# Kernel tuning notes

Measured on AMD Instinct MI355X. Metric: run time of the kernel, lower is better.

The kernel has to match this reference:

```python
import jax, jax.numpy as jnp
import numpy as np

B, L, D, N = 32, 2048, 1024, 16
N_ITERS = 4
EPS = 1e-8
RMS_EPS = 1e-6
H = 2 * D  # SwiGLU hidden


def setup_inputs() -> dict:
    key = jax.random.key(0)
    ks = jax.random.split(key, 16)
    w = lambda i, shape: jax.random.normal(ks[i], shape, dtype=jnp.float32) * 0.02
    return {
        "encoder_output": jax.random.normal(ks[0], (B, L, D), dtype=jnp.float32),
        "slots_noise": jax.random.normal(ks[1], (B, N, D), dtype=jnp.float32),
        "slots_mu": w(2, (1, 1, D)),
        "slots_sigma": jnp.abs(w(3, (1, 1, D))),
        "g_in": jnp.ones((D,), jnp.float32),     # norm_input.weight
        "g_slots": jnp.ones((D,), jnp.float32),  # norm_slots.weight
        "Wq": w(4, (D, D)),   # torch Linear weight layout (out, in)
        "Wk": w(5, (D, D)),
        "Wv": w(6, (D, D)),
        "w1": w(7, (H, D)),
        "w2": w(8, (H, D)),
        "w3": w(9, (D, H)),
        "W_ih": w(10, (3 * D, D)),  # GRUCell weight_ih (r,z,n stacked)
        "W_hh": w(11, (3 * D, D)),
        "b_ih": jnp.zeros((3 * D,), jnp.float32),
        "b_hh": jnp.zeros((3 * D,), jnp.float32),
    }


def _rmsnorm(x, g):
    var = jnp.mean(x * x, axis=-1, keepdims=True)
    return x * jax.lax.rsqrt(var + RMS_EPS) * g


def _gru_cell(x, h, W_ih, W_hh, b_ih, b_hh):
    # torch.nn.GRUCell: gates ordered (r, z, n)
    gi = x @ W_ih.T + b_ih   # [..., 3D]
    gh = h @ W_hh.T + b_hh
    gi_r, gi_z, gi_n = jnp.split(gi, 3, axis=-1)
    gh_r, gh_z, gh_n = jnp.split(gh, 3, axis=-1)
    r = jax.nn.sigmoid(gi_r + gh_r)
    z = jax.nn.sigmoid(gi_z + gh_z)
    n = jnp.tanh(gi_n + r * gh_n)
    return (1.0 - z) * n + z * h


def reference(encoder_output, slots_noise, slots_mu, slots_sigma, g_in, g_slots,
              Wq, Wk, Wv, w1, w2, w3, W_ih, W_hh, b_ih, b_hh):
    d = encoder_output.shape[-1]
    scale = d ** (-0.5)

    inputs = _rmsnorm(encoder_output, g_in)          # [B, L, D]
    k = inputs @ Wk.T                                # [B, L, D]
    v = inputs @ Wv.T                                # [B, L, D]

    slots = slots_mu + slots_sigma * slots_noise     # [B, N, D]

    for _ in range(N_ITERS):
        slots_prev = slots
        s = _rmsnorm(slots, g_slots)                 # [B, N, D]
        q = s @ Wq.T                                 # [B, N, D]
        dots = jnp.einsum('bnd,bld->bnl', q, k) * scale   # [B, N, L]
        attn = jax.nn.softmax(dots, axis=1)          # competitive softmax over slots
        updates = jnp.einsum('bnl,bld->bnd', attn + EPS, v)     # [B, N, D]
        updates = updates / (jnp.sum(attn, axis=-1, keepdims=True) + EPS)
        # SwiGLU
        updates = (jax.nn.silu(updates @ w1.T) * (updates @ w2.T)) @ w3.T
        slots = _gru_cell(updates, slots_prev, W_ih, W_hh, b_ih, b_hh)
    return slots
```

## Files before the change

### kernel.cpp

```cpp
#include <hip/hip_runtime.h>
#include <hip/hip_bf16.h>
#include <stdint.h>


typedef __bf16 bf16;
typedef __bf16 bf16x4 __attribute__((ext_vector_type(4)));
typedef __bf16 bf16x8 __attribute__((ext_vector_type(8)));
typedef float  f32x2  __attribute__((ext_vector_type(2)));
typedef float  f32x4  __attribute__((ext_vector_type(4)));

#define MFMA16(a,b,c) __builtin_amdgcn_mfma_f32_16x16x32_bf16((a),(b),(c),0,0,0)

__device__ __forceinline__ void gload16(const void* g, void* l) {
  __builtin_amdgcn_global_load_lds((__attribute__((address_space(1))) const void*)g,
                                   (__attribute__((address_space(3))) void*)l, 16, 0, 0);
}

template<int OUT_F32>
__device__ __forceinline__ void g64(const bf16* __restrict__ A, const bf16* __restrict__ B,
                                    void* __restrict__ C, int N, int K,
                                    int brow, int bcol, bf16* As, bf16* Bs)
{
  const int tid = threadIdx.x, wave = tid >> 6, lane = tid & 63;
  const int wm = wave >> 1, wn = wave & 1;
  const int r8 = lane >> 3, c8 = (lane & 7) * 8;
  const int cl = lane & 15, rh = lane >> 4;
  f32x4 acc[2][2] = {};

  const bf16* pa0 = A + (size_t)(brow + wave * 16 + r8) * K + c8;
  const bf16* pa1 = A + (size_t)(brow + wave * 16 + 8 + r8) * K + c8;
  const bf16* pb0 = B + (size_t)(bcol + wave * 16 + r8) * K + c8;
  const bf16* pb1 = B + (size_t)(bcol + wave * 16 + 8 + r8) * K + c8;

  auto ST = [&](int T) {
    const int k0 = T * 64, s = T % 3;
    gload16(pa0 + k0, As + s * 4096 + (wave * 16) * 64);
    gload16(pa1 + k0, As + s * 4096 + (wave * 16 + 8) * 64);
    gload16(pb0 + k0, Bs + s * 4096 + (wave * 16) * 64);
    gload16(pb1 + k0, Bs + s * 4096 + (wave * 16 + 8) * 64);
  };

  const int nt = K >> 6;
  ST(0);
  ST(1);
#pragma unroll 3
  for (int t = 0; t < nt; ++t) {
    __builtin_amdgcn_s_barrier();
    if (t + 2 < nt) {
      ST(t + 2);
      asm volatile("s_waitcnt vmcnt(8)" ::: "memory");
    } else if (t + 1 < nt) {
      asm volatile("s_waitcnt vmcnt(4)" ::: "memory");
    } else {
      asm volatile("s_waitcnt vmcnt(0)" ::: "memory");
    }
    __builtin_amdgcn_sched_barrier(0);
    __builtin_amdgcn_s_barrier();
    const int s = t % 3;
#pragma unroll
    for (int kk = 0; kk < 2; ++kk) {
      bf16x8 af[2], bfv[2];
#pragma unroll
      for (int m = 0; m < 2; ++m)
        af[m] = *(const bf16x8*)(As + s * 4096 + (wm * 32 + m * 16 + cl) * 64 + kk * 32 + rh * 8);
#pragma unroll
      for (int n = 0; n < 2; ++n)
        bfv[n] = *(const bf16x8*)(Bs + s * 4096 + (wn * 32 + n * 16 + cl) * 64 + kk * 32 + rh * 8);
#pragma unroll
      for (int m = 0; m < 2; ++m)
#pragma unroll
        for (int n = 0; n < 2; ++n)
          acc[m][n] = MFMA16(af[m], bfv[n], acc[m][n]);
    }
  }

#pragma unroll
  for (int m = 0; m < 2; ++m)
#pragma unroll
    for (int n = 0; n < 2; ++n) {
      int row0 = brow + wm * 32 + m * 16 + rh * 4;
      int col  = bcol + wn * 32 + n * 16 + cl;
#pragma unroll
      for (int r = 0; r < 4; ++r) {
        if (OUT_F32) ((float*)C)[(size_t)(row0 + r) * N + col] = acc[m][n][r];
        else         ((bf16*)C)[(size_t)(row0 + r) * N + col] = (bf16)acc[m][n][r];
      }
    }
}

template<int OUT_F32>
__global__ __launch_bounds__(256, 3)
void gemm_bt64(const bf16* __restrict__ A0, const bf16* __restrict__ B0, void* __restrict__ C0,
               const bf16* __restrict__ A1, const bf16* __restrict__ B1, void* __restrict__ C1,
               int N, int K0, int K1, float* zbuf)
{
  __shared__ __align__(16) bf16 As[3 * 4096];
  __shared__ __align__(16) bf16 Bs[3 * 4096];
  if (zbuf != nullptr && blockIdx.x == 0 && blockIdx.y == 0 && blockIdx.z == 0) {
    zbuf[threadIdx.x] = 0.f;
    zbuf[threadIdx.x + 256] = 0.f;
  }
  const bf16* A = blockIdx.z ? A1 : A0;
  const bf16* B = blockIdx.z ? B1 : B0;
  void* C = blockIdx.z ? C1 : C0;
  const int K = blockIdx.z ? K1 : K0;
  g64<OUT_F32>(A, B, C, N, K, blockIdx.y * 64, blockIdx.x * 64, As, Bs);
}

__device__ __forceinline__ void g128(const bf16* __restrict__ A, const bf16* __restrict__ B,
                                     bf16* __restrict__ C, int N, int K,
                                     int brow, int bcol, bf16* As, bf16* Bs)
{
  const int tid  = threadIdx.x;
  const int wave = tid >> 6, lane = tid & 63;
  const int wm = wave >> 1, wn = wave & 1;
  const int r_a = lane >> 3, c_a = (lane & 7) * 8;
  const int cl = lane & 15, rh = lane >> 4;

  f32x4 acc[4][4] = {};

  for (int k0 = 0; k0 < K; k0 += 64) {
    __syncthreads();
#pragma unroll
    for (int i = 0; i < 4; ++i) {
      gload16(A + (size_t)(brow + i * 32 + wave * 8 + r_a) * K + k0 + c_a, &As[(i * 32 + wave * 8) * 64]);
      gload16(B + (size_t)(bcol + i * 32 + wave * 8 + r_a) * K + k0 + c_a, &Bs[(i * 32 + wave * 8) * 64]);
    }
    __syncthreads();
#pragma unroll
    for (int kk = 0; kk < 2; ++kk) {
      bf16x8 af[4], bfv[4];
#pragma unroll
      for (int m = 0; m < 4; ++m)
        af[m] = *(const bf16x8*)&As[(wm * 64 + m * 16 + cl) * 64 + kk * 32 + rh * 8];
#pragma unroll
      for (int n = 0; n < 4; ++n)
        bfv[n] = *(const bf16x8*)&Bs[(wn * 64 + n * 16 + cl) * 64 + kk * 32 + rh * 8];
#pragma unroll
      for (int m = 0; m < 4; ++m)
#pragma unroll
        for (int n = 0; n < 4; ++n)
          acc[m][n] = MFMA16(af[m], bfv[n], acc[m][n]);
    }
  }
#pragma unroll
  for (int m = 0; m < 4; ++m)
#pragma unroll
    for (int n = 0; n < 4; ++n) {
      int row0 = brow + wm * 64 + m * 16 + rh * 4;
      int col  = bcol + wn * 64 + n * 16 + cl;
#pragma unroll
      for (int r = 0; r < 4; ++r)
        C[(size_t)(row0 + r) * N + col] = (bf16)acc[m][n][r];
    }
}

__global__ __launch_bounds__(256, 2)
void gemm_pre128(const bf16* __restrict__ wkT, const bf16* __restrict__ wqT, bf16* __restrict__ qm_w,
                 const bf16* __restrict__ w12, const bf16* __restrict__ wvT, bf16* __restrict__ w12v,
                 const bf16* __restrict__ wih, const bf16* __restrict__ w3T, bf16* __restrict__ wih3)
{
  __shared__ __align__(16) bf16 As[128 * 64];
  __shared__ __align__(16) bf16 Bs[128 * 64];
  const int id = blockIdx.x;
  if (id < 64)        g128(wkT, wqT, qm_w, 1024, 1024, (id >> 3) * 128, (id & 7) * 128, As, Bs);
  else if (id < 320) { int t = id - 64;  g128(w12, wvT, w12v, 1024, 1024, (t >> 3) * 128, (t & 7) * 128, As, Bs); }
  else               { int t = id - 320; g128(wih, w3T, wih3, 2048, 1024, (t >> 4) * 128, (t & 15) * 128, As, Bs); }
}

__global__ __launch_bounds__(256, 3)
void gemm_swiglu(const bf16* __restrict__ A, const bf16* __restrict__ B12, bf16* __restrict__ G)
{
  __shared__ __align__(16) bf16 As[2][64 * 64];
  __shared__ __align__(16) bf16 B1s[2][64 * 64];
  __shared__ __align__(16) bf16 B2s[2][64 * 64];
  const int tid = threadIdx.x, wave = tid >> 6, lane = tid & 63;
  const int wm = wave >> 1, wn = wave & 1;
  const int brow = blockIdx.y * 64, bcol = blockIdx.x * 64;
  const int r8 = lane >> 3, c8 = (lane & 7) * 8;
  const int cl = lane & 15, rh = lane >> 4;
  f32x4 acc1[2][2] = {}, acc2[2][2] = {};

  const bf16* pa0 = A   + (size_t)(brow + wave * 16 + r8) * 1024 + c8;
  const bf16* pa1 = A   + (size_t)(brow + wave * 16 + 8 + r8) * 1024 + c8;
  const bf16* p10 = B12 + (size_t)(bcol + wave * 16 + r8) * 1024 + c8;
  const bf16* p11 = B12 + (size_t)(bcol + wave * 16 + 8 + r8) * 1024 + c8;
  const bf16* p20 = B12 + (size_t)(2048 + bcol + wave * 16 + r8) * 1024 + c8;
  const bf16* p21 = B12 + (size_t)(2048 + bcol + wave * 16 + 8 + r8) * 1024 + c8;

#define STSW(T) {                                                   \
    int k0_ = (T) * 64, s_ = (T) & 1;                               \
    gload16(pa0 + k0_, &As[s_][(wave * 16) * 64]);                  \
    gload16(pa1 + k0_, &As[s_][(wave * 16 + 8) * 64]);              \
    gload16(p10 + k0_, &B1s[s_][(wave * 16) * 64]);                 \
    gload16(p11 + k0_, &B1s[s_][(wave * 16 + 8) * 64]);             \
    gload16(p20 + k0_, &B2s[s_][(wave * 16) * 64]);                 \
    gload16(p21 + k0_, &B2s[s_][(wave * 16 + 8) * 64]);             \
  }

  STSW(0)
  for (int t = 0; t < 16; ++t) {
    if (t < 15) {
      STSW(t + 1)
      asm volatile("s_waitcnt vmcnt(6)" ::: "memory");
    } else {
      asm volatile("s_waitcnt vmcnt(0)" ::: "memory");
    }
    __builtin_amdgcn_sched_barrier(0);
    __builtin_amdgcn_s_barrier();
    __builtin_amdgcn_sched_barrier(0);
    const int s = t & 1;
#pragma unroll
    for (int kk = 0; kk < 2; ++kk) {
      bf16x8 af[2], b1v[2], b2v[2];
#pragma unroll
      for (int m = 0; m < 2; ++m)
        af[m] = *(const bf16x8*)&As[s][(wm * 32 + m * 16 + cl) * 64 + kk * 32 + rh * 8];
#pragma unroll
      for (int n = 0; n < 2; ++n) {
        b1v[n] = *(const bf16x8*)&B1s[s][(wn * 32 + n * 16 + cl) * 64 + kk * 32 + rh * 8];
        b2v[n] = *(const bf16x8*)&B2s[s][(wn * 32 + n * 16 + cl) * 64 + kk * 32 + rh * 8];
      }
#pragma unroll
      for (int m = 0; m < 2; ++m)
#pragma unroll
        for (int n = 0; n < 2; ++n) {
          acc1[m][n] = MFMA16(af[m], b1v[n], acc1[m][n]);
          acc2[m][n] = MFMA16(af[m], b2v[n], acc2[m][n]);
        }
    }
    __builtin_amdgcn_sched_barrier(0);
    __builtin_amdgcn_s_barrier();
    __builtin_amdgcn_sched_barrier(0);
  }
#undef STSW

#pragma unroll
  for (int m = 0; m < 2; ++m)
#pragma unroll
    for (int n = 0; n < 2; ++n) {
      int row0 = brow + wm * 32 + m * 16 + rh * 4;
      int col  = bcol + wn * 32 + n * 16 + cl;
#pragma unroll
      for (int r = 0; r < 4; ++r) {
        float h1 = acc1[m][n][r], h2 = acc2[m][n][r];
        G[(size_t)(row0 + r) * 2048 + col] = (bf16)(h1 / (1.f + __expf(-h1)) * h2);
      }
    }
}

__global__ __launch_bounds__(256, 2)
void fused_attn(const bf16* __restrict__ qm, const bf16* __restrict__ x,
                bf16* __restrict__ part, float* __restrict__ attn_sum)
{
  extern __shared__ __align__(16) char smem[];
  char* ss  = smem;
  char* ksl = smem + 32768;
  float* p_lds = (float*)(smem + 65536);

  const int lc = blockIdx.x, b = blockIdx.y;
  const int tid = threadIdx.x, wave = tid >> 6, lane = tid & 63;
  const int cl = lane & 15, rh = lane >> 4;

  const bf16* sb = qm + (size_t)b * 16 * 1024;
  {
    const int c16 = tid & 127, row2 = tid >> 7;
#pragma unroll
    for (int i = 0; i < 8; ++i) {
      int row = i * 2 + row2;
      int colb = (c16 * 16) ^ ((row & 7) << 4);
      gload16(sb + row * 1024 + colb / 2, ss + i * 4096 + wave * 1024);
    }
  }

  const bf16* kb = x + ((size_t)b * 2048 + lc * 128) * 1024;
  const int ksw  = ((lane & 7) ^ ((lane >> 3) & 7)) * 8;
  const int krow = wave * 8 + (lane >> 3);

#define STAGE_KS(KT) {                                                            \
    char* d_ = ksl + ((KT) & 1) * 16384;                                          \
    _Pragma("unroll")                                                             \
    for (int i = 0; i < 4; ++i)                                                   \
      gload16(kb + (size_t)(i * 32 + krow) * 1024 + (KT) * 64 + ksw,              \
              d_ + (i * 32 + wave * 8) * 128);                                    \
  }

  f32x4 acc[2] = {};
  STAGE_KS(0)
  for (int kt = 0; kt < 16; ++kt) {
    if (kt < 15) { STAGE_KS(kt + 1) }
    __builtin_amdgcn_sched_barrier(0);
    if (kt < 15) asm volatile("s_waitcnt vmcnt(4)" ::: "memory");
    else         asm volatile("s_waitcnt vmcnt(0)" ::: "memory");
    __builtin_amdgcn_sched_barrier(0);
    __builtin_amdgcn_s_barrier();
    const char* sbuf = ksl + (kt & 1) * 16384;
#pragma unroll
    for (int kk = 0; kk < 2; ++kk) {
      bf16x8 af = *(const bf16x8*)(ss + cl * 2048 +
                    ((kt * 128 + kk * 64 + rh * 16) ^ ((cl & 7) << 4)));
#pragma unroll
      for (int n = 0; n < 2; ++n) {
        int row = wave * 32 + n * 16 + cl;
        bf16x8 bfv = *(const bf16x8*)(sbuf + row * 128 +
                      ((kk * 64 + rh * 16) ^ ((row & 7) << 4)));
        acc[n] = MFMA16(af, bfv, acc[n]);
      }
    }
    __builtin_amdgcn_s_barrier();
    __builtin_amdgcn_sched_barrier(0);
  }
#undef STAGE_KS

  const float scale = 0.03125f;
  float rs[4] = {0.f, 0.f, 0.f, 0.f};
#pragma unroll
  for (int n = 0; n < 2; ++n) {
    float xv[4];
#pragma unroll
    for (int r = 0; r < 4; ++r) xv[r] = acc[n][r] * scale;
    float mx = fmaxf(fmaxf(xv[0], xv[1]), fmaxf(xv[2], xv[3]));
    mx = fmaxf(mx, __shfl_xor(mx, 16));
    mx = fmaxf(mx, __shfl_xor(mx, 32));
    float e[4], sm = 0.f;
#pragma unroll
    for (int r = 0; r < 4; ++r) { e[r] = __expf(xv[r] - mx); sm += e[r]; }
    sm += __shfl_xor(sm, 16);
    sm += __shfl_xor(sm, 32);
    float inv = 1.f / sm;
    f32x4 pk;
#pragma unroll
    for (int r = 0; r < 4; ++r) { float av = e[r] * inv; rs[r] += av; pk[r] = av; }
    int ll = wave * 32 + n * 16 + cl;
    *(f32x4*)&p_lds[ll * 20 + rh * 4] = pk;
  }
#pragma unroll
  for (int off = 1; off < 16; off <<= 1) {
#pragma unroll
    for (int r = 0; r < 4; ++r) rs[r] += __shfl_xor(rs[r], off);
  }
  if (cl == 0) {
#pragma unroll
    for (int r = 0; r < 4; ++r) atomicAdd(&attn_sum[b * 16 + rh * 4 + r], rs[r]);
  }
  __syncthreads();

  const bf16* vb = x + ((size_t)b * 2048 + lc * 128) * 1024 + tid * 4;
  f32x2 pacc2[8][4] = {};
  for (int l = 0; l < 128; ++l) {
    bf16x4 vv = *(const bf16x4*)(vb + (size_t)l * 1024);
    f32x2 xs[4];
#pragma unroll
    for (int j = 0; j < 4; ++j) { float f = (float)vv[j]; xs[j][0] = f; xs[j][1] = f; }
    f32x2 p2[8];
#pragma unroll
    for (int sp = 0; sp < 8; ++sp) p2[sp] = *(const f32x2*)&p_lds[l * 20 + sp * 2];
#pragma unroll
    for (int sp = 0; sp < 8; ++sp)
#pragma unroll
      for (int j = 0; j < 4; ++j)
        pacc2[sp][j] += p2[sp] * xs[j];
  }
  bf16* pb = part + ((size_t)(lc * 32 + b) * 16) * 1024 + tid * 4;
#pragma unroll
  for (int n = 0; n < 16; ++n) {
    bf16x4 o;
#pragma unroll
    for (int r = 0; r < 4; ++r) o[r] = (bf16)pacc2[n >> 1][r][n & 1];
    *(bf16x4*)(pb + (size_t)n * 1024) = o;
  }
}

__global__ void updates_finalize(const bf16* __restrict__ part, const float* __restrict__ attn_sum,
                                 bf16* __restrict__ updraw)
{
  int idx8 = (blockIdx.x * 256 + threadIdx.x) * 8;
  int m = idx8 >> 10;
  float s[8] = {};
#pragma unroll
  for (int ls = 0; ls < 16; ++ls) {
    bf16x8 v = *(const bf16x8*)(part + idx8 + (size_t)ls * 524288);
#pragma unroll
    for (int j = 0; j < 8; ++j) s[j] += (float)v[j];
  }
  float inv = 1.f / (attn_sum[m] + 1e-8f);
  bf16x8 o;
#pragma unroll
  for (int j = 0; j < 8; ++j) o[j] = (bf16)(s[j] * inv);
  *(bf16x8*)(updraw + idx8) = o;
}

__global__ __launch_bounds__(256)
void gru_pw_fused(const float* __restrict__ gi, const float* __restrict__ gh,
                  const float* __restrict__ bih, const float* __restrict__ bhh,
                  const float* __restrict__ g_sl,
                  float* __restrict__ slots, bf16* __restrict__ slots_bf,
                  bf16* __restrict__ s_bf, float* __restrict__ outp)
{
  const int m = blockIdx.x, tid = threadIdx.x;
  const int d0 = tid * 4;
  const size_t base = (size_t)m * 3072 + d0;
  f32x4 gir = *(const f32x4*)(gi + base),        ghr = *(const f32x4*)(gh + base);
  f32x4 giz = *(const f32x4*)(gi + base + 1024), ghz = *(const f32x4*)(gh + base + 1024);
  f32x4 gin = *(const f32x4*)(gi + base + 2048), ghn = *(const f32x4*)(gh + base + 2048);
  f32x4 br  = *(const f32x4*)(bih + d0),        bhr = *(const f32x4*)(bhh + d0);
  f32x4 bz  = *(const f32x4*)(bih + 1024 + d0), bhz = *(const f32x4*)(bhh + 1024 + d0);
  f32x4 bn  = *(const f32x4*)(bih + 2048 + d0), bhn = *(const f32x4*)(bhh + 2048 + d0);
  f32x4 h   = *(const f32x4*)(slots + (size_t)m * 1024 + d0);
  float o[4]; float ssum = 0.f;
#pragma unroll
  for (int j = 0; j < 4; ++j) {
    float r  = gir[j] + br[j] + ghr[j] + bhr[j];
    float z  = giz[j] + bz[j] + ghz[j] + bhz[j];
    float nn = gin[j] + bn[j];
    float hn = ghn[j] + bhn[j];
    r = 1.f / (1.f + expf(-r));
    z = 1.f / (1.f + expf(-z));
    nn = tanhf(nn + r * hn);
    o[j] = (1.f - z) * nn + z * h[j];
    ssum += o[j] * o[j];
  }
#pragma unroll
  for (int off = 32; off; off >>= 1) ssum += __shfl_xor(ssum, off);
  __shared__ float red[4];
  if ((tid & 63) == 0) red[tid >> 6] = ssum;
  __syncthreads();
  float tot = red[0] + red[1] + red[2] + red[3];
  float rsc = rsqrtf(tot * (1.f / 1024.f) + 1e-6f);
  f32x4 gv = *(const f32x4*)(g_sl + d0);
  f32x4 of; bf16x4 ob, sb;
#pragma unroll
  for (int j = 0; j < 4; ++j) { of[j] = o[j]; ob[j] = (bf16)o[j]; sb[j] = (bf16)(o[j] * rsc * gv[j]); }
  *(f32x4*)(slots + (size_t)m * 1024 + d0) = of;
  *(f32x4*)(outp  + (size_t)m * 1024 + d0) = of;
  *(bf16x4*)(slots_bf + (size_t)m * 1024 + d0) = ob;
  *(bf16x4*)(s_bf     + (size_t)m * 1024 + d0) = sb;
}

__global__ __launch_bounds__(256)
void init_slots_fused(const float* __restrict__ noise, const float* __restrict__ mu,
                      const float* __restrict__ sigma, const float* __restrict__ g_sl,
                      float* __restrict__ slots, bf16* __restrict__ slots_bf,
                      bf16* __restrict__ s_bf)
{
  const int m = blockIdx.x, tid = threadIdx.x;
  const int d0 = tid * 4;
  f32x4 nz = *(const f32x4*)(noise + (size_t)m * 1024 + d0);
  f32x4 mv = *(const f32x4*)(mu + d0);
  f32x4 sg = *(const f32x4*)(sigma + d0);
  float o[4]; float ssum = 0.f;
#pragma unroll
  for (int j = 0; j < 4; ++j) { o[j] = mv[j] + sg[j] * nz[j]; ssum += o[j] * o[j]; }
#pragma unroll
  for (int off = 32; off; off >>= 1) ssum += __shfl_xor(ssum, off);
  __shared__ float red[4];
  if ((tid & 63) == 0) red[tid >> 6] = ssum;
  __syncthreads();
  float tot = red[0] + red[1] + red[2] + red[3];
  float rsc = rsqrtf(tot * (1.f / 1024.f) + 1e-6f);
  f32x4 gv = *(const f32x4*)(g_sl + d0);
  f32x4 of; bf16x4 ob, sb;
#pragma unroll
  for (int j = 0; j < 4; ++j) { of[j] = o[j]; ob[j] = (bf16)o[j]; sb[j] = (bf16)(o[j] * rsc * gv[j]); }
  *(f32x4*)(slots + (size_t)m * 1024 + d0) = of;
  *(bf16x4*)(slots_bf + (size_t)m * 1024 + d0) = ob;
  *(bf16x4*)(s_bf     + (size_t)m * 1024 + d0) = sb;
}

__global__ __launch_bounds__(256)
void rmsnorm_cast(const float* __restrict__ x, const float* __restrict__ g, bf16* __restrict__ y)
{
  const int row = blockIdx.x, tid = threadIdx.x;
  float4 xv = ((const float4*)(x + (size_t)row * 1024))[tid];
  float ss = xv.x * xv.x + xv.y * xv.y + xv.z * xv.z + xv.w * xv.w;
#pragma unroll
  for (int off = 32; off; off >>= 1) ss += __shfl_xor(ss, off);
  __shared__ float red[4];
  if ((tid & 63) == 0) red[tid >> 6] = ss;
  __syncthreads();
  float tot = red[0] + red[1] + red[2] + red[3];
  float rs = rsqrtf(tot * (1.f / 1024.f) + 1e-6f);
  float4 gv = ((const float4*)g)[tid];
  bf16x4 o;
  o[0] = (bf16)(xv.x * rs * gv.x); o[1] = (bf16)(xv.y * rs * gv.y);
  o[2] = (bf16)(xv.z * rs * gv.z); o[3] = (bf16)(xv.w * rs * gv.w);
  *(bf16x4*)(y + (size_t)row * 1024 + tid * 4) = o;
}

__global__ __launch_bounds__(256)
void transpose_all(const float* __restrict__ Wq, const float* __restrict__ Wk,
                   const float* __restrict__ Wv, const float* __restrict__ w3,
                   bf16* __restrict__ wqT, bf16* __restrict__ wkT,
                   bf16* __restrict__ wvT, bf16* __restrict__ w3T)
{
  __shared__ float tile[32][33];
  const int z = blockIdx.z;
  const float* in; bf16* out; int R, C;
  if      (z == 0) { in = Wq; out = wqT; R = 1024; C = 1024; }
  else if (z == 1) { in = Wk; out = wkT; R = 1024; C = 1024; }
  else if (z == 2) { in = Wv; out = wvT; R = 1024; C = 1024; }
  else             { in = w3; out = w3T; R = 1024; C = 2048; }
  const int bx = blockIdx.x * 32, by = blockIdx.y * 32;
  if (bx >= C) return;
  const int tx = threadIdx.x & 31, ty = threadIdx.x >> 5;
#pragma unroll
  for (int i = 0; i < 32; i += 8)
    tile[ty + i][tx] = in[(size_t)(by + ty + i) * C + bx + tx];
  __syncthreads();
#pragma unroll
  for (int i = 0; i < 32; i += 8)
    out[(size_t)(bx + ty + i) * R + by + tx] = (bf16)tile[tx][ty + i];
}

__global__ void cast_all(const float* __restrict__ w1, const float* __restrict__ w2,
                         const float* __restrict__ Wih, const float* __restrict__ Whh,
                         bf16* __restrict__ w12_bf, bf16* __restrict__ wih_bf,
                         bf16* __restrict__ whh_b)
{
  int i = (blockIdx.x * 256 + threadIdx.x) * 4;
  const float* src; bf16* dst; int o;
  if      (i < 2097152)  { src = w1;  dst = w12_bf; o = i; }
  else if (i < 4194304)  { src = w2;  dst = w12_bf + 2097152; o = i - 2097152; }
  else if (i < 7340032)  { src = Wih; dst = wih_bf; o = i - 4194304; }
  else                   { src = Whh; dst = whh_b;  o = i - 7340032; }
  float4 v = *(const float4*)(src + o);
  bf16x4 ov; ov[0] = (bf16)v.x; ov[1] = (bf16)v.y; ov[2] = (bf16)v.z; ov[3] = (bf16)v.w;
  *(bf16x4*)(dst + o) = ov;
}

extern "C" void kernel_launch(void* const* d_in, const int* in_sizes, int n_in,
                              void* d_out, int out_size, void* d_ws, size_t ws_size,
                              hipStream_t stream)
{
  const float* enc    = (const float*)d_in[0];
  const float* noise  = (const float*)d_in[1];
  const float* mu     = (const float*)d_in[2];
  const float* sigma  = (const float*)d_in[3];
  const float* g_in   = (const float*)d_in[4];
  const float* g_sl   = (const float*)d_in[5];
  const float* Wq     = (const float*)d_in[6];
  const float* Wk     = (const float*)d_in[7];
  const float* Wv     = (const float*)d_in[8];
  const float* w1     = (const float*)d_in[9];
  const float* w2     = (const float*)d_in[10];
  const float* w3     = (const float*)d_in[11];
  const float* Wih    = (const float*)d_in[12];
  const float* Whh    = (const float*)d_in[13];
  const float* bih    = (const float*)d_in[14];
  const float* bhh    = (const float*)d_in[15];

  char* p = (char*)d_ws;
  auto alloc = [&](size_t bytes) { char* r = p; p += (bytes + 255) & ~(size_t)255; return (void*)r; };

  bf16* inputs  = (bf16*)alloc((size_t)32 * 2048 * 1024 * 2);
  bf16* qm_w    = (bf16*)alloc((size_t)1024 * 1024 * 2);
  bf16* wqT_b   = (bf16*)alloc((size_t)1024 * 1024 * 2);
  bf16* wkT_b   = (bf16*)alloc((size_t)1024 * 1024 * 2);
  bf16* wvT_b   = (bf16*)alloc((size_t)1024 * 1024 * 2);
  bf16* w3T_b   = (bf16*)alloc((size_t)2048 * 1024 * 2);
  bf16* w12_bf  = (bf16*)alloc((size_t)4096 * 1024 * 2);
  bf16* w12v    = (bf16*)alloc((size_t)4096 * 1024 * 2);
  bf16* wih_bf  = (bf16*)alloc((size_t)3072 * 1024 * 2);
  bf16* wih3_b  = (bf16*)alloc((size_t)3072 * 2048 * 2);
  bf16* whh_b   = (bf16*)alloc((size_t)3072 * 1024 * 2);
  float* slots  = (float*)alloc(512 * 1024 * 4);
  bf16* slots_bf= (bf16*)alloc(512 * 1024 * 2);
  bf16* s_bf    = (bf16*)alloc(512 * 1024 * 2);
  bf16* qm_bf   = (bf16*)alloc(512 * 1024 * 2);
  float* attn_sum = (float*)alloc(32 * 16 * 4);
  bf16* part    = (bf16*)alloc((size_t)16 * 512 * 1024 * 2);
  bf16* updraw  = (bf16*)alloc(512 * 1024 * 2);
  bf16* g_bf    = (bf16*)alloc((size_t)512 * 2048 * 2);
  float* gif    = (float*)alloc((size_t)512 * 3072 * 4);
  float* ghf    = (float*)alloc((size_t)512 * 3072 * 4);

  transpose_all<<<dim3(64, 32, 4), 256, 0, stream>>>(Wq, Wk, Wv, w3, wqT_b, wkT_b, wvT_b, w3T_b);
  cast_all<<<10240, 256, 0, stream>>>(w1, w2, Wih, Whh, w12_bf, wih_bf, whh_b);
  gemm_pre128<<<704, 256, 0, stream>>>(wkT_b, wqT_b, qm_w, w12_bf, wvT_b, w12v, wih_bf, w3T_b, wih3_b);

  rmsnorm_cast<<<65536, 256, 0, stream>>>(enc, g_in, inputs);
  init_slots_fused<<<512, 256, 0, stream>>>(noise, mu, sigma, g_sl, slots, slots_bf, s_bf);

  hipFuncSetAttribute(reinterpret_cast<const void*>(fused_attn),
                      hipFuncAttributeMaxDynamicSharedMemorySize, 75776);

  for (int it = 0; it < 4; ++it) {
    gemm_bt64<0><<<dim3(16, 8, 1), 256, 0, stream>>>(s_bf, qm_w, qm_bf, s_bf, qm_w, qm_bf,
                                                     1024, 1024, 1024, attn_sum);
    fused_attn<<<dim3(16, 32), 256, 75776, stream>>>(qm_bf, inputs, part, attn_sum);
    updates_finalize<<<256, 256, 0, stream>>>(part, attn_sum, updraw);
    gemm_swiglu<<<dim3(32, 8), 256, 0, stream>>>(updraw, w12v, g_bf);
    gemm_bt64<1><<<dim3(48, 8, 2), 256, 0, stream>>>(g_bf, wih3_b, gif, slots_bf, whh_b, ghf,
                                                     3072, 2048, 1024, nullptr);
    float* outp = (it == 3) ? (float*)d_out : slots;
    gru_pw_fused<<<512, 256, 0, stream>>>(gif, ghf, bih, bhh, g_sl, slots, slots_bf, s_bf, outp);
  }
}
```

Measured before the change: 669.9 us.

## Fuse iteration loop into one cooperative persistent kernel with grid syncs

Replaces the 24 per-iteration kernel launches with a single cooperative persistent kernel. It loops over the four slot iterations and separates the q-GEMM, attention, finalize, SwiGLU, GRU GEMMs and GRU pointwise stages with grid-wide syncs, using work-stealing style strided loops over tiles. The goal is to remove launch gaps and tail effects between small stages. In exchange, it adds grid barrier costs, caps the grid at occupancy-limited block counts (smem raised to 64KB shared), and keeps a fallback to the multi-kernel path if the cooperative launch fails.

Result: slower. 2.089 ms (+211.8%).

```diff
diff --git a/kernel.cpp b/kernel.cpp
--- a/kernel.cpp
+++ b/kernel.cpp
@@ -1,7 +1,10 @@
 #include <hip/hip_runtime.h>
+#include <hip/hip_cooperative_groups.h>
 #include <hip/hip_bf16.h>
 #include <stdint.h>
 
+
+namespace cg = cooperative_groups;
 
 typedef __bf16 bf16;
 typedef __bf16 bf16x4 __attribute__((ext_vector_type(4)));
@@ -88,25 +91,6 @@
     }
 }
 
-template<int OUT_F32>
-__global__ __launch_bounds__(256, 3)
-void gemm_bt64(const bf16* __restrict__ A0, const bf16* __restrict__ B0, void* __restrict__ C0,
-               const bf16* __restrict__ A1, const bf16* __restrict__ B1, void* __restrict__ C1,
-               int N, int K0, int K1, float* zbuf)
-{
-  __shared__ __align__(16) bf16 As[3 * 4096];
-  __shared__ __align__(16) bf16 Bs[3 * 4096];
-  if (zbuf != nullptr && blockIdx.x == 0 && blockIdx.y == 0 && blockIdx.z == 0) {
-    zbuf[threadIdx.x] = 0.f;
-    zbuf[threadIdx.x + 256] = 0.f;
-  }
-  const bf16* A = blockIdx.z ? A1 : A0;
-  const bf16* B = blockIdx.z ? B1 : B0;
-  void* C = blockIdx.z ? C1 : C0;
-  const int K = blockIdx.z ? K1 : K0;
-  g64<OUT_F32>(A, B, C, N, K, blockIdx.y * 64, blockIdx.x * 64, As, Bs);
-}
-
 __device__ __forceinline__ void g128(const bf16* __restrict__ A, const bf16* __restrict__ B,
                                      bf16* __restrict__ C, int N, int K,
                                      int brow, int bcol, bf16* As, bf16* Bs)
@@ -168,15 +152,14 @@
   else               { int t = id - 320; g128(wih, w3T, wih3, 2048, 1024, (t >> 4) * 128, (t & 15) * 128, As, Bs); }
 }
 
-__global__ __launch_bounds__(256, 3)
-void gemm_swiglu(const bf16* __restrict__ A, const bf16* __restrict__ B12, bf16* __restrict__ G)
-{
-  __shared__ __align__(16) bf16 As[2][64 * 64];
-  __shared__ __align__(16) bf16 B1s[2][64 * 64];
-  __shared__ __align__(16) bf16 B2s[2][64 * 64];
+__device__ __forceinline__ void swiglu_body(const bf16* __restrict__ A, const bf16* __restrict__ B12,
+                                            bf16* __restrict__ G, int brow, int bcol, char* smem)
+{
+  bf16* As  = (bf16*)smem;
+  bf16* B1s = (bf16*)(smem + 16384);
+  bf16* B2s = (bf16*)(smem + 32768);
   const int tid = threadIdx.x, wave = tid >> 6, lane = tid & 63;
   const int wm = wave >> 1, wn = wave & 1;
-  const int brow = blockIdx.y * 64, bcol = blockIdx.x * 64;
   const int r8 = lane >> 3, c8 = (lane & 7) * 8;
   const int cl = lane & 15, rh = lane >> 4;
   f32x4 acc1[2][2] = {}, acc2[2][2] = {};
@@ -188,20 +171,20 @@
   const bf16* p20 = B12 + (size_t)(2048 + bcol + wave * 16 + r8) * 1024 + c8;
   const bf16* p21 = B12 + (size_t)(2048 + bcol + wave * 16 + 8 + r8) * 1024 + c8;
 
-#define STSW(T) {                                                   \
-    int k0_ = (T) * 64, s_ = (T) & 1;                               \
-    gload16(pa0 + k0_, &As[s_][(wave * 16) * 64]);                  \
-    gload16(pa1 + k0_, &As[s_][(wave * 16 + 8) * 64]);              \
-    gload16(p10 + k0_, &B1s[s_][(wave * 16) * 64]);                 \
-    gload16(p11 + k0_, &B1s[s_][(wave * 16 + 8) * 64]);             \
-    gload16(p20 + k0_, &B2s[s_][(wave * 16) * 64]);                 \
-    gload16(p21 + k0_, &B2s[s_][(wave * 16 + 8) * 64]);             \
-  }
-
-  STSW(0)
+  auto ST = [&](int T) {
+    const int k0 = T * 64, s = T & 1;
+    gload16(pa0 + k0, As  + s * 4096 + (wave * 16) * 64);
+    gload16(pa1 + k0, As  + s * 4096 + (wave * 16 + 8) * 64);
+    gload16(p10 + k0, B1s + s * 4096 + (wave * 16) * 64);
+    gload16(p11 + k0, B1s + s * 4096 + (wave * 16 + 8) * 64);
+    gload16(p20 + k0, B2s + s * 4096 + (wave * 16) * 64);
+    gload16(p21 + k0, B2s + s * 4096 + (wave * 16 + 8) * 64);
+  };
+
+  ST(0);
   for (int t = 0; t < 16; ++t) {
     if (t < 15) {
-      STSW(t + 1)
+      ST(t + 1);
       asm volatile("s_waitcnt vmcnt(6)" ::: "memory");
     } else {
       asm volatile("s_waitcnt vmcnt(0)" ::: "memory");
@@ -215,11 +198,11 @@
       bf16x8 af[2], b1v[2], b2v[2];
 #pragma unroll
       for (int m = 0; m < 2; ++m)
-        af[m] = *(const bf16x8*)&As[s][(wm * 32 + m * 16 + cl) * 64 + kk * 32 + rh * 8];
+        af[m] = *(const bf16x8*)(As + s * 4096 + (wm * 32 + m * 16 + cl) * 64 + kk * 32 + rh * 8);
 #pragma unroll
       for (int n = 0; n < 2; ++n) {
-        b1v[n] = *(const bf16x8*)&B1s[s][(wn * 32 + n * 16 + cl) * 64 + kk * 32 + rh * 8];
-        b2v[n] = *(const bf16x8*)&B2s[s][(wn * 32 + n * 16 + cl) * 64 + kk * 32 + rh * 8];
+        b1v[n] = *(const bf16x8*)(B1s + s * 4096 + (wn * 32 + n * 16 + cl) * 64 + kk * 32 + rh * 8);
+        b2v[n] = *(const bf16x8*)(B2s + s * 4096 + (wn * 32 + n * 16 + cl) * 64 + kk * 32 + rh * 8);
       }
 #pragma unroll
       for (int m = 0; m < 2; ++m)
@@ -233,7 +216,6 @@
     __builtin_amdgcn_s_barrier();
     __builtin_amdgcn_sched_barrier(0);
   }
-#undef STSW
 
 #pragma unroll
   for (int m = 0; m < 2; ++m)
@@ -249,16 +231,14 @@
     }
 }
 
-__global__ __launch_bounds__(256, 2)
-void fused_attn(const bf16* __restrict__ qm, const bf16* __restrict__ x,
-                bf16* __restrict__ part, float* __restrict__ attn_sum)
-{
-  extern __shared__ __align__(16) char smem[];
+__device__ __forceinline__ void attn_body(const bf16* __restrict__ qm, const bf16* __restrict__ x,
+                                          bf16* __restrict__ part, float* __restrict__ attn_sum,
+                                          int lc, int b, char* smem)
+{
   char* ss  = smem;
   char* ksl = smem + 32768;
-  float* p_lds = (float*)(smem + 65536);
-
-  const int lc = blockIdx.x, b = blockIdx.y;
+  float* p_lds = (float*)smem;
+
   const int tid = threadIdx.x, wave = tid >> 6, lane = tid & 63;
   const int cl = lane & 15, rh = lane >> 4;
 
@@ -277,18 +257,18 @@
   const int ksw  = ((lane & 7) ^ ((lane >> 3) & 7)) * 8;
   const int krow = wave * 8 + (lane >> 3);
 
-#define STAGE_KS(KT) {                                                            \
-    char* d_ = ksl + ((KT) & 1) * 16384;                                          \
-    _Pragma("unroll")                                                             \
-    for (int i = 0; i < 4; ++i)                                                   \
-      gload16(kb + (size_t)(i * 32 + krow) * 1024 + (KT) * 64 + ksw,              \
-              d_ + (i * 32 + wave * 8) * 128);                                    \
-  }
+  auto STAGE_KS = [&](int KT) {
+    char* d_ = ksl + (KT & 1) * 16384;
+#pragma unroll
+    for (int i = 0; i < 4; ++i)
+      gload16(kb + (size_t)(i * 32 + krow) * 1024 + KT * 64 + ksw,
+              d_ + (i * 32 + wave * 8) * 128);
+  };
 
   f32x4 acc[2] = {};
-  STAGE_KS(0)
+  STAGE_KS(0);
   for (int kt = 0; kt < 16; ++kt) {
-    if (kt < 15) { STAGE_KS(kt + 1) }
+    if (kt < 15) STAGE_KS(kt + 1);
     __builtin_amdgcn_sched_barrier(0);
     if (kt < 15) asm volatile("s_waitcnt vmcnt(4)" ::: "memory");
     else         asm volatile("s_waitcnt vmcnt(0)" ::: "memory");
@@ -310,7 +290,6 @@
     __builtin_amdgcn_s_barrier();
     __builtin_amdgcn_sched_barrier(0);
   }
-#undef STAGE_KS
 
   const float scale = 0.03125f;
   float rs[4] = {0.f, 0.f, 0.f, 0.f};
@@ -371,33 +350,15 @@
   }
 }
 
-__global__ void updates_finalize(const bf16* __restrict__ part, const float* __restrict__ attn_sum,
-                                 bf16* __restrict__ updraw)
-{
-  int idx8 = (blockIdx.x * 256 + threadIdx.x) * 8;
-  int m = idx8 >> 10;
-  float s[8] = {};
-#pragma unroll
-  for (int ls = 0; ls < 16; ++ls) {
-    bf16x8 v = *(const bf16x8*)(part + idx8 + (size_t)ls * 524288);
-#pragma unroll
-    for (int j = 0; j < 8; ++j) s[j] += (float)v[j];
-  }
-  float inv = 1.f / (attn_sum[m] + 1e-8f);
-  bf16x8 o;
-#pragma unroll
-  for (int j = 0; j < 8; ++j) o[j] = (bf16)(s[j] * inv);
-  *(bf16x8*)(updraw + idx8) = o;
-}
-
-__global__ __launch_bounds__(256)
-void gru_pw_fused(const float* __restrict__ gi, const float* __restrict__ gh,
-                  const float* __restrict__ bih, const float* __restrict__ bhh,
-                  const float* __restrict__ g_sl,
-                  float* __restrict__ slots, bf16* __restrict__ slots_bf,
-                  bf16* __restrict__ s_bf, float* __restrict__ outp)
-{
-  const int m = blockIdx.x, tid = threadIdx.x;
+__device__ __forceinline__ void gru_pw_body(const float* __restrict__ gi, const float* __restrict__ gh,
+                                            const float* __restrict__ bih, const float* __restrict__ bhh,
+                                            const float* __restrict__ g_sl,
+                                            float* __restrict__ slots, bf16* __restrict__ slots_bf,
+                                            bf16* __restrict__ s_bf, float* __restrict__ outp,
+                                            int m, char* smem)
+{
+  float* red = (float*)smem;
+  const int tid = threadIdx.x;
   const int d0 = tid * 4;
   const size_t base = (size_t)m * 3072 + d0;
   f32x4 gir = *(const f32x4*)(gi + base),        ghr = *(const f32x4*)(gh + base);
@@ -422,7 +383,6 @@
   }
 #pragma unroll
   for (int off = 32; off; off >>= 1) ssum += __shfl_xor(ssum, off);
-  __shared__ float red[4];
   if ((tid & 63) == 0) red[tid >> 6] = ssum;
   __syncthreads();
   float tot = red[0] + red[1] + red[2] + red[3];
@@ -437,34 +397,143 @@
   *(bf16x4*)(s_bf     + (size_t)m * 1024 + d0) = sb;
 }
 
+__device__ __forceinline__ void finalize_unit(const bf16* __restrict__ part,
+                                              const float* __restrict__ attn_sum,
+                                              bf16* __restrict__ updraw, int u)
+{
+  int idx8 = u * 8, m = idx8 >> 10;
+  float s[8] = {};
+#pragma unroll
+  for (int ls = 0; ls < 16; ++ls) {
+    bf16x8 v = *(const bf16x8*)(part + idx8 + (size_t)ls * 524288);
+#pragma unroll
+    for (int j = 0; j < 8; ++j) s[j] += (float)v[j];
+  }
+  float inv = 1.f / (attn_sum[m] + 1e-8f);
+  bf16x8 o;
+#pragma unroll
+  for (int j = 0; j < 8; ++j) o[j] = (bf16)(s[j] * inv);
+  *(bf16x8*)(updraw + idx8) = o;
+}
+
+__global__ __launch_bounds__(256, 2)
+void mega_loop(const bf16* __restrict__ qm_w, bf16* __restrict__ qm_bf,
+               bf16* __restrict__ s_bf, const bf16* __restrict__ x,
+               bf16* __restrict__ part, float* __restrict__ attn_sum,
+               bf16* __restrict__ updraw, const bf16* __restrict__ w12v,
+               bf16* __restrict__ g_bf, const bf16* __restrict__ wih3,
+               const bf16* __restrict__ whh, float* __restrict__ gif,
+               float* __restrict__ ghf, float* __restrict__ slots,
+               bf16* __restrict__ slots_bf, const float* __restrict__ bih,
+               const float* __restrict__ bhh, const float* __restrict__ g_sl,
+               float* __restrict__ dout)
+{
+  extern __shared__ __align__(16) char smem[];
+  cg::grid_group grid = cg::this_grid();
+  const int blk = blockIdx.x, tid = threadIdx.x, nb = gridDim.x;
+
+  for (int it = 0; it < 4; ++it) {
+    if (blk == 0) { attn_sum[tid] = 0.f; attn_sum[tid + 256] = 0.f; }
+    for (int u = blk; u < 128; u += nb) {
+      g64<0>(s_bf, qm_w, qm_bf, 1024, 1024, (u >> 4) * 64, (u & 15) * 64,
+             (bf16*)smem, (bf16*)(smem + 24576));
+      __syncthreads();
+    }
+    __threadfence();
+    grid.sync();
+
+    for (int u = blk; u < 512; u += nb) {
+      attn_body(qm_bf, x, part, attn_sum, u & 15, u >> 4, smem);
+      __syncthreads();
+    }
+    __threadfence();
+    grid.sync();
+
+    for (int u = blk * 256 + tid; u < 65536; u += nb * 256)
+      finalize_unit(part, attn_sum, updraw, u);
+    __threadfence();
+    grid.sync();
+
+    for (int u = blk; u < 256; u += nb) {
+      swiglu_body(updraw, w12v, g_bf, (u >> 5) * 64, (u & 31) * 64, smem);
+      __syncthreads();
+    }
+    __threadfence();
+    grid.sync();
+
+    for (int u = blk; u < 768; u += nb) {
+      if (u < 384)
+        g64<1>(g_bf, wih3, gif, 3072, 2048, (u / 48) * 64, (u % 48) * 64,
+               (bf16*)smem, (bf16*)(smem + 24576));
+      else {
+        int t = u - 384;
+        g64<1>(slots_bf, whh, ghf, 3072, 1024, (t / 48) * 64, (t % 48) * 64,
+               (bf16*)smem, (bf16*)(smem + 24576));
+      }
+      __syncthreads();
+    }
+    __threadfence();
+    grid.sync();
+
+    float* outp = (it == 3) ? dout : slots;
+    for (int u = blk; u < 512; u += nb) {
+      gru_pw_body(gif, ghf, bih, bhh, g_sl, slots, slots_bf, s_bf, outp, u, smem);
+      __syncthreads();
+    }
+    __threadfence();
+    grid.sync();
+  }
+}
+
+template<int OUT_F32>
+__global__ __launch_bounds__(256, 3)
+void gemm_bt64(const bf16* __restrict__ A0, const bf16* __restrict__ B0, void* __restrict__ C0,
+               const bf16* __restrict__ A1, const bf16* __restrict__ B1, void* __restrict__ C1,
+               int N, int K0, int K1, float* zbuf)
+{
+  __shared__ __align__(16) bf16 As[3 * 4096];
+  __shared__ __align__(16) bf16 Bs[3 * 4096];
+  if (zbuf != nullptr && blockIdx.x == 0 && blockIdx.y == 0 && blockIdx.z == 0) {
+    zbuf[threadIdx.x] = 0.f;
+    zbuf[threadIdx.x + 256] = 0.f;
+  }
+  const bf16* A = blockIdx.z ? A1 : A0;
+  const bf16* B = blockIdx.z ? B1 : B0;
+  void* C = blockIdx.z ? C1 : C0;
+  const int K = blockIdx.z ? K1 : K0;
+  g64<OUT_F32>(A, B, C, N, K, blockIdx.y * 64, blockIdx.x * 64, As, Bs);
+}
+
+__global__ __launch_bounds__(256, 2)
+void k_attn(const bf16* __restrict__ qm, const bf16* __restrict__ x,
+            bf16* __restrict__ part, float* __restrict__ attn_sum)
+{
+  extern __shared__ __align__(16) char smem[];
+  attn_body(qm, x, part, attn_sum, blockIdx.x, blockIdx.y, smem);
+}
+
+__global__ void k_finalize(const bf16* __restrict__ part, const float* __restrict__ attn_sum,
+                           bf16* __restrict__ updraw)
+{
+  finalize_unit(part, attn_sum, updraw, blockIdx.x * 256 + threadIdx.x);
+}
+
+__global__ __launch_bounds__(256, 3)
+void k_swiglu(const bf16* __restrict__ A, const bf16* __restrict__ B12, bf16* __restrict__ G)
+{
+  __shared__ __align__(16) char smem[49152];
+  swiglu_body(A, B12, G, blockIdx.y * 64, blockIdx.x * 64, smem);
+}
+
 __global__ __launch_bounds__(256)
-void init_slots_fused(const float* __restrict__ noise, const float* __restrict__ mu,
-                      const float* __restrict__ sigma, const float* __restrict__ g_sl,
-                      float* __restrict__ slots, bf16* __restrict__ slots_bf,
-                      bf16* __restrict__ s_bf)
-{
-  const int m = blockIdx.x, tid = threadIdx.x;
-  const int d0 = tid * 4;
-  f32x4 nz = *(const f32x4*)(noise + (size_t)m * 1024 + d0);
-  f32x4 mv = *(const f32x4*)(mu + d0);
-  f32x4 sg = *(const f32x4*)(sigma + d0);
-  float o[4]; float ssum = 0.f;
-#pragma unroll
-  for (int j = 0; j < 4; ++j) { o[j] = mv[j] + sg[j] * nz[j]; ssum += o[j] * o[j]; }
-#pragma unroll
-  for (int off = 32; off; off >>= 1) ssum += __shfl_xor(ssum, off);
-  __shared__ float red[4];
-  if ((tid & 63) == 0) red[tid >> 6] = ssum;
-  __syncthreads();
-  float tot = red[0] + red[1] + red[2] + red[3];
-  float rsc = rsqrtf(tot * (1.f / 1024.f) + 1e-6f);
-  f32x4 gv = *(const f32x4*)(g_sl + d0);
-  f32x4 of; bf16x4 ob, sb;
-#pragma unroll
-  for (int j = 0; j < 4; ++j) { of[j] = o[j]; ob[j] = (bf16)o[j]; sb[j] = (bf16)(o[j] * rsc * gv[j]); }
-  *(f32x4*)(slots + (size_t)m * 1024 + d0) = of;
-  *(bf16x4*)(slots_bf + (size_t)m * 1024 + d0) = ob;
-  *(bf16x4*)(s_bf     + (size_t)m * 1024 + d0) = sb;
+void k_gru_pw(const float* __restrict__ gi, const float* __restrict__ gh,
+              const float* __restrict__ bih, const float* __restrict__ bhh,
+              const float* __restrict__ g_sl, float* __restrict__ slots,
+              bf16* __restrict__ slots_bf, bf16* __restrict__ s_bf,
+              float* __restrict__ outp)
+{
+  __shared__ __align__(16) char smem[64];
+  gru_pw_body(gi, gh, bih, bhh, g_sl, slots, slots_bf, s_bf, outp, blockIdx.x, smem);
 }
 
 __global__ __launch_bounds__(256)
@@ -485,6 +554,36 @@
   o[0] = (bf16)(xv.x * rs * gv.x); o[1] = (bf16)(xv.y * rs * gv.y);
   o[2] = (bf16)(xv.z * rs * gv.z); o[3] = (bf16)(xv.w * rs * gv.w);
   *(bf16x4*)(y + (size_t)row * 1024 + tid * 4) = o;
+}
+
+__global__ __launch_bounds__(256)
+void init_slots_fused(const float* __restrict__ noise, const float* __restrict__ mu,
+                      const float* __restrict__ sigma, const float* __restrict__ g_sl,
+                      float* __restrict__ slots, bf16* __restrict__ slots_bf,
+                      bf16* __restrict__ s_bf)
+{
+  const int m = blockIdx.x, tid = threadIdx.x;
+  const int d0 = tid * 4;
+  f32x4 nz = *(const f32x4*)(noise + (size_t)m * 1024 + d0);
+  f32x4 mv = *(const f32x4*)(mu + d0);
+  f32x4 sg = *(const f32x4*)(sigma + d0);
+  float o[4]; float ssum = 0.f;
+#pragma unroll
+  for (int j = 0; j < 4; ++j) { o[j] = mv[j] + sg[j] * nz[j]; ssum += o[j] * o[j]; }
+#pragma unroll
+  for (int off = 32; off; off >>= 1) ssum += __shfl_xor(ssum, off);
+  __shared__ float red[4];
+  if ((tid & 63) == 0) red[tid >> 6] = ssum;
+  __syncthreads();
+  float tot = red[0] + red[1] + red[2] + red[3];
+  float rsc = rsqrtf(tot * (1.f / 1024.f) + 1e-6f);
+  f32x4 gv = *(const f32x4*)(g_sl + d0);
+  f32x4 of; bf16x4 ob, sb;
+#pragma unroll
+  for (int j = 0; j < 4; ++j) { of[j] = o[j]; ob[j] = (bf16)o[j]; sb[j] = (bf16)(o[j] * rsc * gv[j]); }
+  *(f32x4*)(slots + (size_t)m * 1024 + d0) = of;
+  *(bf16x4*)(slots_bf + (size_t)m * 1024 + d0) = ob;
+  *(bf16x4*)(s_bf     + (size_t)m * 1024 + d0) = sb;
 }
 
 __global__ __launch_bounds__(256)
@@ -573,6 +672,7 @@
   bf16* g_bf    = (bf16*)alloc((size_t)512 * 2048 * 2);
   float* gif    = (float*)alloc((size_t)512 * 3072 * 4);
   float* ghf    = (float*)alloc((size_t)512 * 3072 * 4);
+  float* doutp  = (float*)d_out;
 
   transpose_all<<<dim3(64, 32, 4), 256, 0, stream>>>(Wq, Wk, Wv, w3, wqT_b, wkT_b, wvT_b, w3T_b);
   cast_all<<<10240, 256, 0, stream>>>(w1, w2, Wih, Whh, w12_bf, wih_bf, whh_b);
@@ -581,18 +681,40 @@
   rmsnorm_cast<<<65536, 256, 0, stream>>>(enc, g_in, inputs);
   init_slots_fused<<<512, 256, 0, stream>>>(noise, mu, sigma, g_sl, slots, slots_bf, s_bf);
 
-  hipFuncSetAttribute(reinterpret_cast<const void*>(fused_attn),
-                      hipFuncAttributeMaxDynamicSharedMemorySize, 75776);
-
-  for (int it = 0; it < 4; ++it) {
-    gemm_bt64<0><<<dim3(16, 8, 1), 256, 0, stream>>>(s_bf, qm_w, qm_bf, s_bf, qm_w, qm_bf,
-                                                     1024, 1024, 1024, attn_sum);
-    fused_attn<<<dim3(16, 32), 256, 75776, stream>>>(qm_bf, inputs, part, attn_sum);
-    updates_finalize<<<256, 256, 0, stream>>>(part, attn_sum, updraw);
-    gemm_swiglu<<<dim3(32, 8), 256, 0, stream>>>(updraw, w12v, g_bf);
-    gemm_bt64<1><<<dim3(48, 8, 2), 256, 0, stream>>>(g_bf, wih3_b, gif, slots_bf, whh_b, ghf,
-                                                     3072, 2048, 1024, nullptr);
-    float* outp = (it == 3) ? (float*)d_out : slots;
-    gru_pw_fused<<<512, 256, 0, stream>>>(gif, ghf, bih, bhh, g_sl, slots, slots_bf, s_bf, outp);
-  }
-}
+  const unsigned SMEM = 65536;
+  hipFuncSetAttribute(reinterpret_cast<const void*>(mega_loop),
+                      hipFuncAttributeMaxDynamicSharedMemorySize, SMEM);
+  int maxB = 0;
+  hipError_t qerr = hipOccupancyMaxActiveBlocksPerMultiprocessor(
+      &maxB, reinterpret_cast<const void*>(mega_loop), 256, SMEM);
+  int nb = (qerr == hipSuccess && maxB > 0) ? maxB * 256 : 0;
+  if (nb > 512) nb = 512;
+
+  hipError_t lerr = hipErrorUnknown;
+  if (nb >= 1) {
+    void* margs[] = {
+      (void*)&qm_w, (void*)&qm_bf, (void*)&s_bf, (void*)&inputs, (void*)&part,
+      (void*)&attn_sum, (void*)&updraw, (void*)&w12v, (void*)&g_bf, (void*)&wih3_b,
+      (void*)&whh_b, (void*)&gif, (void*)&ghf, (void*)&slots, (void*)&slots_bf,
+      (void*)&bih, (void*)&bhh, (void*)&g_sl, (void*)&doutp
+    };
+    lerr = hipLaunchCooperativeKernel(reinterpret_cast<const void*>(mega_loop),
+                                      dim3(nb), dim3(256), margs, SMEM, stream);
+  }
+
+  if (lerr != hipSuccess) {
+    hipFuncSetAttribute(reinterpret_cast<const void*>(k_attn),
+                        hipFuncAttributeMaxDynamicSharedMemorySize, SMEM);
+    for (int it = 0; it < 4; ++it) {
+      gemm_bt64<0><<<dim3(16, 8, 1), 256, 0, stream>>>(s_bf, qm_w, qm_bf, s_bf, qm_w, qm_bf,
+                                                       1024, 1024, 1024, attn_sum);
+      k_attn<<<dim3(16, 32), 256, SMEM, stream>>>(qm_bf, inputs, part, attn_sum);
+      k_finalize<<<256, 256, 0, stream>>>(part, attn_sum, updraw);
+      k_swiglu<<<dim3(32, 8), 256, 0, stream>>>(updraw, w12v, g_bf);
+      gemm_bt64<1><<<dim3(48, 8, 2), 256, 0, stream>>>(g_bf, wih3_b, gif, slots_bf, whh_b, ghf,
+                                                       3072, 2048, 1024, nullptr);
+      float* outp = (it == 3) ? doutp : slots;
+      k_gru_pw<<<512, 256, 0, stream>>>(gif, ghf, bih, bhh, g_sl, slots, slots_bf, s_bf, outp);
+    }
+  }
+}
```
